# Kernel optimization log

Measured on AMD Instinct MI355X. Metric: run time of the kernel, lower is better.

## Reference

```python
import jax, jax.numpy as jnp
import numpy as np

B, T, C, H = 8, 2048, 1024, 128  # batch, seq, embed_dim, head_size

def setup_inputs() -> dict:
    key = jax.random.key(0)
    kx, kk, kq, kv = jax.random.split(key, 4)
    s = 1.0 / np.sqrt(C)  # ~nn.Linear init scale
    return {
        "x": jax.random.normal(kx, (B, T, C), dtype=jnp.float32),
        "Wk": jax.random.normal(kk, (H, C), dtype=jnp.float32) * s,
        "Wq": jax.random.normal(kq, (H, C), dtype=jnp.float32) * s,
        "Wv": jax.random.normal(kv, (H, C), dtype=jnp.float32) * s,
    }

def reference(x, Wk, Wq, Wv):
    b, t, c = x.shape
    # Faithful to source: q uses the KEY projection (bug in original); Wq is unused.
    k = jnp.einsum('btc,hc->bth', x, Wk)   # [B,T,H]
    q = jnp.einsum('btc,hc->bth', x, Wk)   # [B,T,H]  (self.key used for q)
    v = jnp.einsum('btc,hc->bth', x, Wv)   # [B,T,H]
    score = jnp.einsum('bqh,bkh->bqk', q, k) * (c ** -0.5)  # scale by C, per source
    causal = jnp.tril(jnp.ones((t, t), dtype=bool))
    score = jnp.where(causal, score, -jnp.inf)
    attn = jax.nn.softmax(score, axis=-1)   # [B,T,T]
    out = jnp.einsum('bqk,bkh->bqh', attn, v)  # [B,T,H]
    return out
```

## Files before the change

### kernel.cpp

```cpp
#include <hip/hip_runtime.h>
#include <hip/hip_bf16.h>

#define BATCH 8
#define SEQ   2048
#define EMB   1024
#define HD    128

typedef __attribute__((ext_vector_type(8))) short bf16x8;
typedef __attribute__((ext_vector_type(4))) short bf16x4;
typedef __attribute__((ext_vector_type(4))) float f32x4;

__device__ __forceinline__ short f2bf(float f) {
    union { float f; unsigned u; } v; v.f = f;
    unsigned r = v.u + 0x7fffu + ((v.u >> 16) & 1u);
    return (short)(r >> 16);
}


__global__ void prep_w(const float* __restrict__ Wk, const float* __restrict__ Wv,
                       short* __restrict__ Wimg) {
    int g  = blockIdx.x * 256 + threadIdx.x;
    int q  = g & 3;
    int l  = (g >> 2) & 15;
    int f  = (g >> 6) & 7;
    int kk = (g >> 9) & 1;
    int kc = (g >> 10) & 15;
    int nh = (g >> 14) & 1;
    const float* src = (nh ? Wv : Wk) + (size_t)(f * 16 + l) * EMB + kc * 64 + kk * 32 + q * 8;
    float4 f0 = *(const float4*)src;
    float4 f1 = *(const float4*)(src + 4);
    bf16x8 v;
    v[0]=f2bf(f0.x); v[1]=f2bf(f0.y); v[2]=f2bf(f0.z); v[3]=f2bf(f0.w);
    v[4]=f2bf(f1.x); v[5]=f2bf(f1.y); v[6]=f2bf(f1.z); v[7]=f2bf(f1.w);
    *(bf16x8*)&Wimg[(size_t)g * 8] = v;
}

__global__ __launch_bounds__(256, 2)
void proj_kernel(const float* __restrict__ x, const short* __restrict__ Wimg,
                 short* __restrict__ Kimg,
                 short* __restrict__ Vimg)
{
    __shared__ __align__(16) union {
        struct { short A[2][4096]; short B[2][8192]; } st;
        short ep[8192];
    } sm;

    const int tid  = threadIdx.x;
    const int wave = tid >> 6;
    const int lane = tid & 63;
    const int quad = lane >> 4;
    const int l16  = lane & 15;
    const int nh   = blockIdx.x & 1;
    const int mt   = blockIdx.x >> 1;
    const int row0 = mt * 64;

    const int m_st  = tid >> 2;
    const int seg   = tid & 3;
    const int mf_st = m_st >> 4, l_st = m_st & 15;
    const float* xsrc = x + (size_t)(row0 + m_st) * EMB + seg * 16;
    const short* wsrc = Wimg + (size_t)nh * 131072;

    f32x4 acc[4][2];
#pragma unroll
    for (int a = 0; a < 4; ++a)
#pragma unroll
        for (int c = 0; c < 2; ++c) acc[a][c] = f32x4{0.f, 0.f, 0.f, 0.f};

    {
        float4 xv[4];
#pragma unroll
        for (int e = 0; e < 4; ++e) xv[e] = *(const float4*)(xsrc + e * 4);
#pragma unroll
        for (int i = 0; i < 4; ++i)
            *(bf16x8*)&sm.st.B[0][tid * 32 + i * 8] = *(const bf16x8*)&wsrc[tid * 32 + i * 8];
#pragma unroll
        for (int e = 0; e < 4; ++e) {
            int k_in = seg * 16 + e * 4;
            int kk = k_in >> 5, q = (k_in >> 3) & 3, hh = (k_in >> 2) & 1;
            bf16x4 h4 = { f2bf(xv[e].x), f2bf(xv[e].y), f2bf(xv[e].z), f2bf(xv[e].w) };
            *(bf16x4*)&sm.st.A[0][((((mf_st * 2 + kk) * 16 + l_st) * 4 + q) * 8) + hh * 4] = h4;
        }
    }
    __syncthreads();

    for (int kc = 0; kc < 16; ++kc) {
        const int cur = kc & 1, nxt = cur ^ 1;
        float4 xv[4];
        bf16x8 wl[4];
        if (kc < 15) {
            const float* nx = xsrc + (kc + 1) * 64;
#pragma unroll
            for (int e = 0; e < 4; ++e) xv[e] = *(const float4*)(nx + e * 4);
            const short* nw = wsrc + (size_t)(kc + 1) * 8192;
#pragma unroll
            for (int i = 0; i < 4; ++i) wl[i] = *(const bf16x8*)&nw[tid * 32 + i * 8];
        }

#pragma unroll
        for (int kk = 0; kk < 2; ++kk) {
            bf16x8 bfr[2];
#pragma unroll
            for (int f2 = 0; f2 < 2; ++f2)
                bfr[f2] = *(const bf16x8*)&sm.st.B[cur][(((kk * 8 + wave * 2 + f2) * 16 + l16) * 4 + quad) * 8];
#pragma unroll
            for (int mf = 0; mf < 4; ++mf) {
                bf16x8 af = *(const bf16x8*)&sm.st.A[cur][(((mf * 2 + kk) * 16 + l16) * 4 + quad) * 8];
#pragma unroll
                for (int f2 = 0; f2 < 2; ++f2)
                    acc[mf][f2] = __builtin_amdgcn_mfma_f32_16x16x32_bf16(af, bfr[f2], acc[mf][f2], 0, 0, 0);
            }
        }

        if (kc < 15) {
#pragma unroll
            for (int i = 0; i < 4; ++i)
                *(bf16x8*)&sm.st.B[nxt][tid * 32 + i * 8] = wl[i];
#pragma unroll
            for (int e = 0; e < 4; ++e) {
                int k_in = seg * 16 + e * 4;
                int kk = k_in >> 5, q = (k_in >> 3) & 3, hh = (k_in >> 2) & 1;
                bf16x4 h4 = { f2bf(xv[e].x), f2bf(xv[e].y), f2bf(xv[e].z), f2bf(xv[e].w) };
                *(bf16x4*)&sm.st.A[nxt][((((mf_st * 2 + kk) * 16 + l_st) * 4 + q) * 8) + hh * 4] = h4;
            }
        }
        __syncthreads();
    }

#pragma unroll
    for (int mf = 0; mf < 4; ++mf)
#pragma unroll
        for (int f2 = 0; f2 < 2; ++f2)
#pragma unroll
            for (int r = 0; r < 4; ++r) {
                const int row = mf * 16 + quad * 4 + r;
                const int h   = wave * 32 + f2 * 16 + l16;
                int idx;
                if (nh == 0)
                    idx = ((((h >> 5) * 4 + (row >> 4)) * 16 + (row & 15)) * 4 + ((h >> 3) & 3)) * 8 + (h & 7);
                else
                    idx = ((((row >> 5) * 8 + (h >> 4)) * 16 + (h & 15)) * 4 + ((row >> 3) & 3)) * 8 + (row & 7);
                sm.ep[idx] = f2bf(acc[mf][f2][r]);
            }
    __syncthreads();

    {
        short* dst = (nh == 0 ? Kimg : Vimg) + (size_t)mt * 8192 + tid * 32;
#pragma unroll
        for (int i = 0; i < 4; ++i)
            *(bf16x8*)(dst + i * 8) = *(const bf16x8*)&sm.ep[tid * 32 + i * 8];
    }
}

#define LOG2E 1.4426950408889634f

__global__ __launch_bounds__(128, 1)
void attn_kernel(const short* __restrict__ Kimg,
                 const short* __restrict__ Vimg,
                 float* __restrict__ out)
{
    __shared__ __align__(16) short ps[2][1024];

    const int tid  = threadIdx.x;
    const int wave = tid >> 6;
    const int lane = tid & 63;
    const int quad = lane >> 4;
    const int l16  = lane & 15;

    const int b   = blockIdx.x & 7;
    const int qtu = (blockIdx.x >> 3) * 2 + wave;
    const int qt  = (qtu & 1) ? (127 - (qtu >> 1)) : (qtu >> 1);
    const int n   = (qt >> 2) + 1;

    const short* Kb = Kimg + (size_t)b * 32 * 8192;
    const short* Vb = Vimg + (size_t)b * 32 * 8192;

    bf16x8 qf[4];
    {
        const short* qi = Kb + (size_t)(qt >> 2) * 8192;
        const int jsq = qt & 3;
#pragma unroll
        for (int kc = 0; kc < 4; ++kc)
            qf[kc] = *(const bf16x8*)&qi[(((kc * 4 + jsq) * 16 + l16) * 4 + quad) * 8];
    }

    f32x4 O[8];
#pragma unroll
    for (int f = 0; f < 8; ++f) O[f] = f32x4{0.f, 0.f, 0.f, 0.f};
    float lp[4] = {0.f, 0.f, 0.f, 0.f};

    const float coef = LOG2E * 0.03125f;
    short* psw = ps[wave];

    for (int jt = 0; jt < n; ++jt) {
        const short* ki = Kb + (size_t)jt * 8192;
        const short* vi = Vb + (size_t)jt * 8192;

        bf16x8 kfr[16];
#pragma unroll
        for (int kc = 0; kc < 4; ++kc)
#pragma unroll
            for (int js = 0; js < 4; ++js)
                kfr[kc * 4 + js] = *(const bf16x8*)&ki[(((kc * 4 + js) * 16 + l16) * 4 + quad) * 8];

        f32x4 S[4];
#pragma unroll
        for (int js = 0; js < 4; ++js) S[js] = f32x4{0.f, 0.f, 0.f, 0.f};
#pragma unroll
        for (int kc = 0; kc < 4; ++kc)
#pragma unroll
            for (int js = 0; js < 4; ++js)
                S[js] = __builtin_amdgcn_mfma_f32_16x16x32_bf16(qf[kc], kfr[kc * 4 + js], S[js], 0, 0, 0);

        bf16x8 vfr[16];
#pragma unroll
        for (int jc = 0; jc < 2; ++jc)
#pragma unroll
            for (int f = 0; f < 8; ++f)
                vfr[jc * 8 + f] = *(const bf16x8*)&vi[(((jc * 8 + f) * 16 + l16) * 4 + quad) * 8];

        const bool diag = (jt == n - 1);
#pragma unroll
        for (int js = 0; js < 4; ++js) {
            const int jj = jt * 64 + js * 16 + l16;
            const int cb = js * 2 + (l16 >> 3);
            const int e  = l16 & 7;
#pragma unroll
            for (int r = 0; r < 4; ++r) {
                float vv = S[js][r] * coef;
                if (diag && (jj > qt * 16 + quad * 4 + r)) vv = -INFINITY;
                float p = exp2f(vv);
                lp[r] += p;
                const int i8 = quad * 4 + r;
                psw[(i8 * 8 + (cb ^ (i8 & 7))) * 8 + e] = f2bf(p);
            }
        }

#pragma unroll
        for (int jc = 0; jc < 2; ++jc) {
            const int pblk = l16 * 8 + ((jc * 4 + quad) ^ (l16 & 7));
            bf16x8 pa = *(const bf16x8*)&psw[pblk * 8];
#pragma unroll
            for (int f = 0; f < 8; ++f)
                O[f] = __builtin_amdgcn_mfma_f32_16x16x32_bf16(pa, vfr[jc * 8 + f], O[f], 0, 0, 0);
        }
    }

#pragma unroll
    for (int r = 0; r < 4; ++r) {
        float s = lp[r];
        s += __shfl_xor(s, 1);
        s += __shfl_xor(s, 2);
        s += __shfl_xor(s, 4);
        s += __shfl_xor(s, 8);
        lp[r] = s;
    }
#pragma unroll
    for (int r = 0; r < 4; ++r) {
        const float inv = 1.f / lp[r];
        const int row = qt * 16 + quad * 4 + r;
        float* dst = out + (size_t)(b * SEQ + row) * HD + l16;
#pragma unroll
        for (int f = 0; f < 8; ++f)
            dst[f * 16] = O[f][r] * inv;
    }
}

extern "C" void kernel_launch(void* const* d_in, const int* in_sizes, int n_in,
                              void* d_out, int out_size, void* d_ws, size_t ws_size,
                              hipStream_t stream) {
    const float* x  = (const float*)d_in[0];
    const float* Wk = (const float*)d_in[1];
    const float* Wv = (const float*)d_in[3];
    float* out = (float*)d_out;

    short* Wimg = (short*)d_ws;
    short* Kimg = Wimg + (size_t)262144;
    short* Vimg = Kimg + (size_t)BATCH * 32 * 8192;

    prep_w<<<128, 256, 0, stream>>>(Wk, Wv, Wimg);
    proj_kernel<<<512, 256, 0, stream>>>(x, Wimg, Kimg, Vimg);
    attn_kernel<<<512, 128, 0, stream>>>(Kimg, Vimg, out);
}
```

Measured before the change: 164.5 us.

## Split attention KV loop across wave pairs and pad projection A tile

The attention kernel now runs four waves per block. Each query tile is handled by a pair of waves that take alternating key tiles, and their partial outputs and row sums are merged through shared memory before the final normalisation. This doubles the number of waves working on the long causal rows, cutting per-wave serial latency and raising occupancy. The cost is extra shared memory and a block-wide barrier. Separately, the projection kernel stores the x tile in a row-major layout padded to 72 columns, written with wider 16-byte stores, which simplifies the conversion stores and the MFMA A-fragment addressing.

New measurement: 158.0 us. 1.04x faster.

```diff
diff --git a/kernel.cpp b/kernel.cpp
--- a/kernel.cpp
+++ b/kernel.cpp
@@ -7,7 +7,6 @@
 #define HD    128
 
 typedef __attribute__((ext_vector_type(8))) short bf16x8;
-typedef __attribute__((ext_vector_type(4))) short bf16x4;
 typedef __attribute__((ext_vector_type(4))) float f32x4;
 
 __device__ __forceinline__ short f2bf(float f) {
@@ -41,7 +40,7 @@
                  short* __restrict__ Vimg)
 {
     __shared__ __align__(16) union {
-        struct { short A[2][4096]; short B[2][8192]; } st;
+        struct { short A[2][64][72]; short B[2][8192]; } st;
         short ep[8192];
     } sm;
 
@@ -54,10 +53,9 @@
     const int mt   = blockIdx.x >> 1;
     const int row0 = mt * 64;
 
-    const int m_st  = tid >> 2;
-    const int seg   = tid & 3;
-    const int mf_st = m_st >> 4, l_st = m_st & 15;
-    const float* xsrc = x + (size_t)(row0 + m_st) * EMB + seg * 16;
+    const int srow = tid >> 2;
+    const int sseg = tid & 3;
+    const float* xsrc = x + (size_t)(row0 + srow) * EMB + sseg * 16;
     const short* wsrc = Wimg + (size_t)nh * 131072;
 
     f32x4 acc[4][2];
@@ -73,13 +71,13 @@
 #pragma unroll
         for (int i = 0; i < 4; ++i)
             *(bf16x8*)&sm.st.B[0][tid * 32 + i * 8] = *(const bf16x8*)&wsrc[tid * 32 + i * 8];
-#pragma unroll
-        for (int e = 0; e < 4; ++e) {
-            int k_in = seg * 16 + e * 4;
-            int kk = k_in >> 5, q = (k_in >> 3) & 3, hh = (k_in >> 2) & 1;
-            bf16x4 h4 = { f2bf(xv[e].x), f2bf(xv[e].y), f2bf(xv[e].z), f2bf(xv[e].w) };
-            *(bf16x4*)&sm.st.A[0][((((mf_st * 2 + kk) * 16 + l_st) * 4 + q) * 8) + hh * 4] = h4;
-        }
+        bf16x8 v0, v1;
+        v0[0]=f2bf(xv[0].x); v0[1]=f2bf(xv[0].y); v0[2]=f2bf(xv[0].z); v0[3]=f2bf(xv[0].w);
+        v0[4]=f2bf(xv[1].x); v0[5]=f2bf(xv[1].y); v0[6]=f2bf(xv[1].z); v0[7]=f2bf(xv[1].w);
+        v1[0]=f2bf(xv[2].x); v1[1]=f2bf(xv[2].y); v1[2]=f2bf(xv[2].z); v1[3]=f2bf(xv[2].w);
+        v1[4]=f2bf(xv[3].x); v1[5]=f2bf(xv[3].y); v1[6]=f2bf(xv[3].z); v1[7]=f2bf(xv[3].w);
+        *(bf16x8*)&sm.st.A[0][srow][sseg * 16]     = v0;
+        *(bf16x8*)&sm.st.A[0][srow][sseg * 16 + 8] = v1;
     }
     __syncthreads();
 
@@ -104,7 +102,7 @@
                 bfr[f2] = *(const bf16x8*)&sm.st.B[cur][(((kk * 8 + wave * 2 + f2) * 16 + l16) * 4 + quad) * 8];
 #pragma unroll
             for (int mf = 0; mf < 4; ++mf) {
-                bf16x8 af = *(const bf16x8*)&sm.st.A[cur][(((mf * 2 + kk) * 16 + l16) * 4 + quad) * 8];
+                bf16x8 af = *(const bf16x8*)&sm.st.A[cur][mf * 16 + l16][kk * 32 + quad * 8];
 #pragma unroll
                 for (int f2 = 0; f2 < 2; ++f2)
                     acc[mf][f2] = __builtin_amdgcn_mfma_f32_16x16x32_bf16(af, bfr[f2], acc[mf][f2], 0, 0, 0);
@@ -115,13 +113,13 @@
 #pragma unroll
             for (int i = 0; i < 4; ++i)
                 *(bf16x8*)&sm.st.B[nxt][tid * 32 + i * 8] = wl[i];
-#pragma unroll
-            for (int e = 0; e < 4; ++e) {
-                int k_in = seg * 16 + e * 4;
-                int kk = k_in >> 5, q = (k_in >> 3) & 3, hh = (k_in >> 2) & 1;
-                bf16x4 h4 = { f2bf(xv[e].x), f2bf(xv[e].y), f2bf(xv[e].z), f2bf(xv[e].w) };
-                *(bf16x4*)&sm.st.A[nxt][((((mf_st * 2 + kk) * 16 + l_st) * 4 + q) * 8) + hh * 4] = h4;
-            }
+            bf16x8 v0, v1;
+            v0[0]=f2bf(xv[0].x); v0[1]=f2bf(xv[0].y); v0[2]=f2bf(xv[0].z); v0[3]=f2bf(xv[0].w);
+            v0[4]=f2bf(xv[1].x); v0[5]=f2bf(xv[1].y); v0[6]=f2bf(xv[1].z); v0[7]=f2bf(xv[1].w);
+            v1[0]=f2bf(xv[2].x); v1[1]=f2bf(xv[2].y); v1[2]=f2bf(xv[2].z); v1[3]=f2bf(xv[2].w);
+            v1[4]=f2bf(xv[3].x); v1[5]=f2bf(xv[3].y); v1[6]=f2bf(xv[3].z); v1[7]=f2bf(xv[3].w);
+            *(bf16x8*)&sm.st.A[nxt][srow][sseg * 16]     = v0;
+            *(bf16x8*)&sm.st.A[nxt][srow][sseg * 16 + 8] = v1;
         }
         __syncthreads();
     }
@@ -153,12 +151,14 @@
 
 #define LOG2E 1.4426950408889634f
 
-__global__ __launch_bounds__(128, 1)
+__global__ __launch_bounds__(256, 2)
 void attn_kernel(const short* __restrict__ Kimg,
                  const short* __restrict__ Vimg,
                  float* __restrict__ out)
 {
-    __shared__ __align__(16) short ps[2][1024];
+    __shared__ __align__(16) short ps[4][1024];
+    __shared__ float obuf[2][16][132];
+    __shared__ float lbuf[2][16];
 
     const int tid  = threadIdx.x;
     const int wave = tid >> 6;
@@ -166,10 +166,12 @@
     const int quad = lane >> 4;
     const int l16  = lane & 15;
 
-    const int b   = blockIdx.x & 7;
-    const int qtu = (blockIdx.x >> 3) * 2 + wave;
-    const int qt  = (qtu & 1) ? (127 - (qtu >> 1)) : (qtu >> 1);
-    const int n   = (qt >> 2) + 1;
+    const int b    = blockIdx.x & 7;
+    const int g    = blockIdx.x >> 3;
+    const int pair = wave >> 1;
+    const int p    = wave & 1;
+    const int qt   = pair ? (127 - g) : g;
+    const int n    = (qt >> 2) + 1;
 
     const short* Kb = Kimg + (size_t)b * 32 * 8192;
     const short* Vb = Vimg + (size_t)b * 32 * 8192;
@@ -191,7 +193,7 @@
     const float coef = LOG2E * 0.03125f;
     short* psw = ps[wave];
 
-    for (int jt = 0; jt < n; ++jt) {
+    for (int jt = p; jt < n; jt += 2) {
         const short* ki = Kb + (size_t)jt * 8192;
         const short* vi = Vb + (size_t)jt * 8192;
 
@@ -228,10 +230,10 @@
             for (int r = 0; r < 4; ++r) {
                 float vv = S[js][r] * coef;
                 if (diag && (jj > qt * 16 + quad * 4 + r)) vv = -INFINITY;
-                float p = exp2f(vv);
-                lp[r] += p;
+                float pe = exp2f(vv);
+                lp[r] += pe;
                 const int i8 = quad * 4 + r;
-                psw[(i8 * 8 + (cb ^ (i8 & 7))) * 8 + e] = f2bf(p);
+                psw[(i8 * 8 + (cb ^ (i8 & 7))) * 8 + e] = f2bf(pe);
             }
         }
 
@@ -254,14 +256,32 @@
         s += __shfl_xor(s, 8);
         lp[r] = s;
     }
-#pragma unroll
-    for (int r = 0; r < 4; ++r) {
-        const float inv = 1.f / lp[r];
-        const int row = qt * 16 + quad * 4 + r;
-        float* dst = out + (size_t)(b * SEQ + row) * HD + l16;
+
+    if (p == 1) {
 #pragma unroll
         for (int f = 0; f < 8; ++f)
-            dst[f * 16] = O[f][r] * inv;
+#pragma unroll
+            for (int r = 0; r < 4; ++r)
+                obuf[pair][quad * 4 + r][f * 16 + l16] = O[f][r];
+        if (l16 == 0) {
+#pragma unroll
+            for (int r = 0; r < 4; ++r) lbuf[pair][quad * 4 + r] = lp[r];
+        }
+    }
+    __syncthreads();
+
+    if (p == 0) {
+#pragma unroll
+        for (int r = 0; r < 4; ++r) {
+            const int row16 = quad * 4 + r;
+            const float L   = lp[r] + lbuf[pair][row16];
+            const float inv = 1.f / L;
+            const int row   = qt * 16 + row16;
+            float* dst = out + (size_t)(b * SEQ + row) * HD + l16;
+#pragma unroll
+            for (int f = 0; f < 8; ++f)
+                dst[f * 16] = (O[f][r] + obuf[pair][row16][f * 16 + l16]) * inv;
+        }
     }
 }
 
@@ -279,5 +299,5 @@
 
     prep_w<<<128, 256, 0, stream>>>(Wk, Wv, Wimg);
     proj_kernel<<<512, 256, 0, stream>>>(x, Wimg, Kimg, Vimg);
-    attn_kernel<<<512, 128, 0, stream>>>(Kimg, Vimg, out);
-}
+    attn_kernel<<<512, 256, 0, stream>>>(Kimg, Vimg, out);
+}
```
